# Kernel tuning notes

Hardware: AMD Instinct MI355X
Metric: run time of the kernel (lower is better)

## Reference

```python
import jax, jax.numpy as jnp
import numpy as np

B, D, H, C = 32768, 512, 512, 128  # batch, input_dim, hidden, n_classes (nurse==doctor)
L = 3  # 3 PAN layers and 3 shared FC layers
BN_EPS = 1e-5


def setup_inputs() -> dict:
    key = jax.random.key(0)
    ks = iter(jax.random.split(key, 64))

    def rn(shape, scale):
        return (jax.random.normal(next(ks), shape, jnp.float32) * scale)

    inv = lambda fan: 1.0 / np.sqrt(fan)

    x = jax.random.normal(next(ks), (B, D), jnp.float32)
    s_n = jax.random.randint(next(ks), (B,), 0, C)
    s_d = jax.random.randint(next(ks), (B,), 0, C)
    # cols -4 / -3 carry integer staffing caps (s_nurse_max, s_doctor_max)
    x = x.at[:, -4].set(s_n.astype(jnp.float32)).at[:, -3].set(s_d.astype(jnp.float32))

    inp = {
        'x': x,
        # ClinicalPAN params, stacked over L=3 layers (and 3 branches)
        'pbw': rn((L, 3, D, 32), inv(D)), 'pbb': jnp.zeros((L, 3, 32), jnp.float32),
        'paw1': rn((L, D, 64), inv(D)),  'pab1': jnp.zeros((L, 64), jnp.float32),
        'paw2': rn((L, 64, 32), inv(64)),'pab2': jnp.zeros((L, 32), jnp.float32),
        'piw1': rn((L, D, 16), inv(D)),  'pib1': jnp.zeros((L, 16), jnp.float32),
        'piw2': rn((L, 16, 1), inv(16)), 'pib2': jnp.zeros((L, 1), jnp.float32),
        'pfw': rn((L, 96, D), inv(96)),  'pfb': jnp.zeros((L, D), jnp.float32),
        'pgw': rn((L, D, D), inv(D)),    'pgb': jnp.zeros((L, D), jnp.float32),
        # shared Linear + BatchNorm1d (eval mode: running stats), stacked
        'fcw': rn((L, D, H), inv(D)),    'fcb': jnp.zeros((L, H), jnp.float32),
        'bng': jnp.ones((L, H), jnp.float32),  'bnb': jnp.zeros((L, H), jnp.float32),
        'bnm': jnp.zeros((L, H), jnp.float32), 'bnv': jnp.ones((L, H), jnp.float32),
        # heads
        'nhw1': rn((H, 64), inv(H)), 'nhb1': jnp.zeros((64,), jnp.float32),
        'nhw2': rn((64, C), inv(64)), 'nhb2': jnp.zeros((C,), jnp.float32),
        'dhw1': rn((H, 64), inv(H)), 'dhb1': jnp.zeros((64,), jnp.float32),
        'dhw2': rn((64, C), inv(64)), 'dhb2': jnp.zeros((C,), jnp.float32),
        'wtw1': rn((H, 64), inv(H)), 'wtb1': jnp.zeros((64,), jnp.float32),
        'wtw2': rn((64, 1), inv(64)), 'wtb2': jnp.zeros((1,), jnp.float32),
    }
    return inp


def reference(x, pbw, pbb, paw1, pab1, paw2, pab2, piw1, pib1, piw2, pib2,
              pfw, pfb, pgw, pgb, fcw, fcb, bng, bnb, bnm, bnv,
              nhw1, nhb1, nhw2, nhb2, dhw1, dhb1, dhw2, dhb2,
              wtw1, wtb1, wtw2, wtb2):
    # integer caps (constants w.r.t. grad)
    s_n = jax.lax.stop_gradient(x[:, -4]).astype(jnp.int32)
    s_d = jax.lax.stop_gradient(x[:, -3]).astype(jnp.int32)

    h = x
    for l in range(L):  # ClinicalPAN stack (dropout = identity in eval)
        cw = jax.nn.sigmoid(jax.nn.relu(h @ paw1[l] + pab1[l]) @ paw2[l] + pab2[l])   # [B,32]
        ci = jax.nn.sigmoid(jax.nn.relu(h @ piw1[l] + pib1[l]) @ piw2[l] + pib2[l])   # [B,1]
        feats = jax.nn.relu(jnp.einsum('bd,kdh->bkh', h, pbw[l]) + pbb[l][None])      # [B,3,32]
        weighted = feats * (cw * ci)[:, None, :]                                       # [B,3,32]
        fused = weighted.reshape(h.shape[0], 96) @ pfw[l] + pfb[l]                     # [B,D]
        gate = jax.nn.sigmoid(h @ pgw[l] + pgb[l])
        h = fused + gate * h

    for i in range(L):  # shared Linear -> BN(eval) -> ReLU
        z = h @ fcw[i] + fcb[i]
        z = bng[i] * (z - bnm[i]) * jax.lax.rsqrt(bnv[i] + BN_EPS) + bnb[i]
        h = jax.nn.relu(z)

    nurse_logits = jax.nn.relu(h @ nhw1 + nhb1) @ nhw2 + nhb2   # [B,C]
    doctor_logits = jax.nn.relu(h @ dhw1 + dhb1) @ dhw2 + dhb2  # [B,C]
    wait_time = jax.nn.relu(h @ wtw1 + wtb1) @ wtw2 + wtb2      # [B,1]

    idx = jnp.arange(C)
    nm = (idx[None, :] <= s_n[:, None]).astype(nurse_logits.dtype)
    dm = (idx[None, :] <= s_d[:, None]).astype(doctor_logits.dtype)
    NEG = jnp.asarray(-1e9, nurse_logits.dtype)
    nurse_logits = nurse_logits * nm + (1.0 - nm) * NEG
    doctor_logits = doctor_logits * dm + (1.0 - dm) * NEG
    return nurse_logits, doctor_logits, wait_time
```

## Files before the change

### kernel.cpp

```cpp
#include <hip/hip_runtime.h>

#define DI __device__ __forceinline__

typedef short bf16x8 __attribute__((ext_vector_type(8)));
typedef float f32x4  __attribute__((ext_vector_type(4)));

#define MFMA(a,b,c) __builtin_amdgcn_mfma_f32_16x16x32_bf16(a,b,c,0,0,0)

constexpr int    SZ_WT = 512*80;
constexpr int    SZ_WB = 512*96;
constexpr int    SZ_WF = 96*512;
constexpr int    SZ_WG = 512*512;
constexpr int    SZ_WC = 512*512;
constexpr size_t OFF_WT  = 0;
constexpr size_t OFF_WB  = OFF_WT + 3*(size_t)SZ_WT;
constexpr size_t OFF_WF  = OFF_WB + 3*(size_t)SZ_WB;
constexpr size_t OFF_WG  = OFF_WF + 3*(size_t)SZ_WF;
constexpr size_t OFF_WC  = OFF_WG + 3*(size_t)SZ_WG;
constexpr size_t OFF_WH  = OFF_WC + 3*(size_t)SZ_WC;
constexpr size_t OFF_WH2 = OFF_WH + (size_t)512*192;
constexpr size_t WS_TOTAL= OFF_WH2 + (size_t)128*256;

DI short f2b(float f){ unsigned u; __builtin_memcpy(&u,&f,4); u += 0x7fffu + ((u>>16)&1u); return (short)(u>>16); }
DI float b2f(short s){ unsigned u = ((unsigned)(unsigned short)s)<<16; float f; __builtin_memcpy(&f,&u,4); return f; }
DI float sigm(float x){ return 1.f/(1.f+__expf(-x)); }

__global__ __launch_bounds__(256) void prep_weights(
    const float* __restrict__ pbw,  const float* __restrict__ paw1,
    const float* __restrict__ piw1, const float* __restrict__ pfw,
    const float* __restrict__ pgw,  const float* __restrict__ fcw,
    const float* __restrict__ nhw1, const float* __restrict__ nhw2,
    const float* __restrict__ dhw1, const float* __restrict__ dhw2,
    const float* __restrict__ wtw1, short* __restrict__ ws)
{
  size_t t = (size_t)blockIdx.x*256 + threadIdx.x;
  if (t >= WS_TOTAL) return;
  float v = 0.f;
  if (t < OFF_WB) {
    int q=(int)t; int ly=q/SZ_WT; int qq=q%SZ_WT;
    int j=qq&7, lane=(qq>>3)&63, tile=qq>>9, kt=tile&15, nt=tile>>4;
    int k=kt*32+((lane>>4)<<3)+j, n=nt*16+(lane&15);
    v = (n<64) ? paw1[((size_t)ly*512+k)*64+n] : piw1[((size_t)ly*512+k)*16+(n-64)];
  } else if (t < OFF_WF) {
    int q=(int)(t-OFF_WB); int ly=q/SZ_WB; int qq=q%SZ_WB;
    int j=qq&7, lane=(qq>>3)&63, tile=qq>>9, kt=tile&15, nt=tile>>4;
    int k=kt*32+((lane>>4)<<3)+j, c=nt*16+(lane&15);
    v = pbw[(((size_t)ly*3+(c>>5))*512+k)*32+(c&31)];
  } else if (t < OFF_WG) {
    int q=(int)(t-OFF_WF); int ly=q/SZ_WF; int qq=q%SZ_WF;
    int j=qq&7, lane=(qq>>3)&63, tile=qq>>9, kt=tile%3, nt=tile/3;
    int k=kt*32+((lane>>4)<<3)+j, n=nt*16+(lane&15);
    v = pfw[((size_t)ly*96+k)*512+n];
  } else if (t < OFF_WC) {
    int q=(int)(t-OFF_WG); int ly=q/SZ_WG; int qq=q%SZ_WG;
    int j=qq&7, lane=(qq>>3)&63, tile=qq>>9, kt=tile&15, nt=tile>>4;
    int k=kt*32+((lane>>4)<<3)+j, n=nt*16+(lane&15);
    v = pgw[((size_t)ly*512+k)*512+n];
  } else if (t < OFF_WH) {
    int q=(int)(t-OFF_WC); int ly=q/SZ_WC; int qq=q%SZ_WC;
    int j=qq&7, lane=(qq>>3)&63, tile=qq>>9, kt=tile&15, nt=tile>>4;
    int k=kt*32+((lane>>4)<<3)+j, n=nt*16+(lane&15);
    v = fcw[((size_t)ly*512+k)*512+n];
  } else if (t < OFF_WH2) {
    int qq=(int)(t-OFF_WH);
    int j=qq&7, lane=(qq>>3)&63, tile=qq>>9, kt=tile&15, nt=tile>>4;
    int k=kt*32+((lane>>4)<<3)+j, n=nt*16+(lane&15);
    v = (n<64) ? nhw1[(size_t)k*64+n] : (n<128) ? dhw1[(size_t)k*64+(n-64)] : wtw1[(size_t)k*64+(n-128)];
  } else {
    int qq=(int)(t-OFF_WH2);
    int j=qq&7, lane=(qq>>3)&63, tile=qq>>9, kt=tile&3, nt=tile>>2;
    int k=kt*32+((lane>>4)<<3)+j, n=nt*16+(lane&15);
    if (k<64) v = (n<128) ? nhw2[(size_t)k*128+n] : 0.f;
    else      v = (n>=128)? dhw2[(size_t)(k-64)*128+(n-128)] : 0.f;
  }
  ws[t] = f2b(v);
}

__global__ __launch_bounds__(512, 4) void pan_main(
  const float* __restrict__ x,
  const float* __restrict__ pbb,  const float* __restrict__ pab1,
  const float* __restrict__ paw2, const float* __restrict__ pab2,
  const float* __restrict__ pib1, const float* __restrict__ piw2,
  const float* __restrict__ pib2, const float* __restrict__ pfb,
  const float* __restrict__ pgb,  const float* __restrict__ fcb,
  const float* __restrict__ bng,  const float* __restrict__ bnb,
  const float* __restrict__ bnm,  const float* __restrict__ bnv,
  const float* __restrict__ nhb1, const float* __restrict__ nhb2,
  const float* __restrict__ dhb1, const float* __restrict__ dhb2,
  const float* __restrict__ wtb1, const float* __restrict__ wtw2,
  const float* __restrict__ wtb2,
  const short* __restrict__ ws, float* __restrict__ out)
{
  __shared__ __align__(16) char lds[81920];
  char* hA = lds;
  char* hB = lds + 32768;
  char* sU = lds + 65536;
  char* sW = lds + 73728;

  const int tid  = threadIdx.x;
  const int wave = tid >> 6;
  const int l    = tid & 63;
  const int lr   = l & 15;
  const int lb   = l >> 4;
  const int swzA = (lr & 7) << 4;
  const size_t row0 = (size_t)blockIdx.x * 32;

  #pragma unroll 2
  for (int c = tid; c < 2048; c += 512) {
    int row = c >> 6, k0 = (c & 63) << 3;
    const float4* s0 = (const float4*)(x + (row0 + row)*512 + k0);
    float4 f0 = s0[0], f1 = s0[1];
    bf16x8 p;
    p[0]=f2b(f0.x); p[1]=f2b(f0.y); p[2]=f2b(f0.z); p[3]=f2b(f0.w);
    p[4]=f2b(f1.x); p[5]=f2b(f1.y); p[6]=f2b(f1.z); p[7]=f2b(f1.w);
    *(bf16x8*)(hA + row*1024 + ((k0*2) ^ ((row&7)<<4))) = p;
  }
  __syncthreads();

  auto ldA = [&](const char* base, int rt, int kt) -> bf16x8 {
    int row = rt*16 + lr;
    return *(const bf16x8*)(base + row*1024 + ((kt*64 + lb*16) ^ swzA));
  };
  auto ldB = [&](const short* W, int K32, int nt, int kt) -> bf16x8 {
    return *(const bf16x8*)(W + (((size_t)(nt*K32 + kt))*64 + l)*8);
  };
  auto ldH = [&](const char* base, int row, int col) -> float {
    return b2f(*(const short*)(base + row*1024 + ((col*2) ^ ((row&7)<<4))));
  };
  auto stH = [&](char* base, int row, int col, float v) {
    *(short*)(base + row*1024 + ((col*2) ^ ((row&7)<<4))) = f2b(v);
  };
  const f32x4 FZ = {0.f,0.f,0.f,0.f};

  for (int ly = 0; ly < 3; ++ly) {
    if (wave < 5) {
      const short* W = ws + OFF_WT + (size_t)ly*SZ_WT;
      f32x4 acc[2];
      #pragma unroll
      for (int rt=0;rt<2;++rt) acc[rt] = FZ;
      #pragma unroll 2
      for (int kt=0;kt<16;++kt) {
        bf16x8 b = ldB(W,16,wave,kt);
        #pragma unroll
        for (int rt=0;rt<2;++rt) acc[rt] = MFMA(ldA(hA,rt,kt), b, acc[rt]);
      }
      const int col = wave*16 + lr;
      const float bias = (col<64) ? pab1[ly*64+col] : pib1[ly*16+(col-64)];
      #pragma unroll
      for (int rt=0;rt<2;++rt)
        #pragma unroll
        for (int jj=0;jj<4;++jj) {
          int row = rt*16 + lb*4 + jj;
          *(short*)(sU + row*160 + col*2) = f2b(fmaxf(acc[rt][jj]+bias, 0.f));
        }
    }
    __syncthreads();
    if (tid < 32) {
      float s = pib2[ly];
      bf16x8 t0 = *(const bf16x8*)(sU + tid*160 + 128);
      bf16x8 t1 = *(const bf16x8*)(sU + tid*160 + 144);
      #pragma unroll
      for (int i=0;i<8;++i) {
        s += b2f(t0[i]) * piw2[ly*16+i];
        s += b2f(t1[i]) * piw2[ly*16+8+i];
      }
      *(float*)(sU + 5120 + tid*4) = sigm(s);
    }
    __syncthreads();
    {
      const int r = tid>>4, j0 = (tid&15)<<1;
      float a2[2];
      a2[0] = pab2[ly*32 + j0];
      a2[1] = pab2[ly*32 + j0 + 1];
      #pragma unroll 2
      for (int k8=0;k8<8;++k8) {
        bf16x8 tv8 = *(const bf16x8*)(sU + r*160 + k8*16);
        #pragma unroll
        for (int i8=0;i8<8;++i8) {
          float tv = b2f(tv8[i8]);
          float2 wr = *(const float2*)(paw2 + ((size_t)ly*64 + k8*8+i8)*32 + j0);
          a2[0]=fmaf(tv,wr.x,a2[0]); a2[1]=fmaf(tv,wr.y,a2[1]);
        }
      }
      const float civ = *(const float*)(sU + 5120 + r*4);
      *(short*)(sU + 5248 + (r*32 + j0    )*2) = f2b(sigm(a2[0]) * civ);
      *(short*)(sU + 5248 + (r*32 + j0 + 1)*2) = f2b(sigm(a2[1]) * civ);
    }
    __syncthreads();
    if (wave < 6) {
      const short* W = ws + OFF_WB + (size_t)ly*SZ_WB;
      f32x4 acc[2];
      #pragma unroll
      for (int rt=0;rt<2;++rt) acc[rt] = FZ;
      #pragma unroll 2
      for (int kt=0;kt<16;++kt) {
        bf16x8 b = ldB(W,16,wave,kt);
        #pragma unroll
        for (int rt=0;rt<2;++rt) acc[rt] = MFMA(ldA(hA,rt,kt), b, acc[rt]);
      }
      const int col = wave*16 + lr;
      const float bias = pbb[ly*96 + col];
      #pragma unroll
      for (int rt=0;rt<2;++rt)
        #pragma unroll
        for (int jj=0;jj<4;++jj) {
          int row = rt*16 + lb*4 + jj;
          float cc = b2f(*(const short*)(sU + 5248 + (row*32 + (col&31))*2));
          float wv = fmaxf(acc[rt][jj]+bias, 0.f) * cc;
          *(short*)(sW + row*256 + ((col*2) ^ ((row&7)<<4))) = f2b(wv);
        }
    }
    __syncthreads();
    {
      const short* Wg = ws + OFF_WG + (size_t)ly*SZ_WG;
      const short* Wf = ws + OFF_WF + (size_t)ly*SZ_WF;
      #pragma unroll 1
      for (int c=0; c<4; ++c) {
        f32x4 acc[2];
        #pragma unroll
        for (int rt=0;rt<2;++rt) acc[rt] = FZ;
        #pragma unroll 2
        for (int kt=0;kt<16;++kt) {
          bf16x8 b = ldB(Wg,16, wave*4+c, kt);
          #pragma unroll
          for (int rt=0;rt<2;++rt) acc[rt] = MFMA(ldA(hA,rt,kt), b, acc[rt]);
        }
        const int col = (wave*4+c)*16 + lr;
        const float gb = pgb[ly*512+col];
        const float fb = pfb[ly*512+col];
        #pragma unroll
        for (int rt=0;rt<2;++rt)
          #pragma unroll
          for (int jj=0;jj<4;++jj) {
            int row = rt*16 + lb*4 + jj;
            acc[rt][jj] = sigm(acc[rt][jj]+gb)*ldH(hA,row,col) + fb;
          }
        #pragma unroll 1
        for (int kt=0;kt<3;++kt) {
          bf16x8 b = ldB(Wf,3, wave*4+c, kt);
          #pragma unroll
          for (int rt=0;rt<2;++rt) {
            int row = rt*16 + lr;
            bf16x8 a = *(const bf16x8*)(sW + row*256 + ((kt*64 + lb*16) ^ swzA));
            acc[rt] = MFMA(a,b,acc[rt]);
          }
        }
        #pragma unroll
        for (int rt=0;rt<2;++rt)
          #pragma unroll
          for (int jj=0;jj<4;++jj)
            stH(hB, rt*16 + lb*4 + jj, col, acc[rt][jj]);
      }
    }
    __syncthreads();
    { char* t = hA; hA = hB; hB = t; }
  }

  for (int fi=0; fi<3; ++fi) {
    const short* W = ws + OFF_WC + (size_t)fi*SZ_WC;
    #pragma unroll 1
    for (int c=0; c<4; ++c) {
      f32x4 acc[2];
      #pragma unroll
      for (int rt=0;rt<2;++rt) acc[rt] = FZ;
      #pragma unroll 2
      for (int kt=0;kt<16;++kt) {
        bf16x8 b = ldB(W,16, wave*4+c, kt);
        #pragma unroll
        for (int rt=0;rt<2;++rt) acc[rt] = MFMA(ldA(hA,rt,kt), b, acc[rt]);
      }
      const int col = (wave*4+c)*16 + lr;
      const float sc = bng[fi*512+col] * rsqrtf(bnv[fi*512+col] + 1e-5f);
      const float of = bnb[fi*512+col] - bnm[fi*512+col]*sc;
      const float bb = fcb[fi*512+col];
      #pragma unroll
      for (int rt=0;rt<2;++rt)
        #pragma unroll
        for (int jj=0;jj<4;++jj)
          stH(hB, rt*16 + lb*4 + jj, col,
              fmaxf((acc[rt][jj] + bb)*sc + of, 0.f));
    }
    __syncthreads();
    { char* t = hA; hA = hB; hB = t; }
  }

  {
    const short* W = ws + OFF_WH;
    {
      f32x4 acc[2];
      #pragma unroll
      for (int rt=0;rt<2;++rt) acc[rt] = FZ;
      #pragma unroll 2
      for (int kt=0;kt<16;++kt) {
        bf16x8 b = ldB(W,16,wave,kt);
        #pragma unroll
        for (int rt=0;rt<2;++rt) acc[rt] = MFMA(ldA(hA,rt,kt), b, acc[rt]);
      }
      const int col = wave*16 + lr;
      const float bias = (col<64) ? nhb1[col] : dhb1[col-64];
      #pragma unroll
      for (int rt=0;rt<2;++rt)
        #pragma unroll
        for (int jj=0;jj<4;++jj) {
          int row = rt*16 + lb*4 + jj;
          *(short*)(hB + row*384 + ((col*2) ^ ((row&7)<<4))) =
              f2b(fmaxf(acc[rt][jj]+bias, 0.f));
        }
    }
    if (wave < 4) {
      f32x4 acc[2];
      #pragma unroll
      for (int rt=0;rt<2;++rt) acc[rt] = FZ;
      #pragma unroll 2
      for (int kt=0;kt<16;++kt) {
        bf16x8 b = ldB(W,16, 8+wave, kt);
        #pragma unroll
        for (int rt=0;rt<2;++rt) acc[rt] = MFMA(ldA(hA,rt,kt), b, acc[rt]);
      }
      const int col = (8+wave)*16 + lr;
      const float bias = wtb1[col-128];
      #pragma unroll
      for (int rt=0;rt<2;++rt)
        #pragma unroll
        for (int jj=0;jj<4;++jj) {
          int row = rt*16 + lb*4 + jj;
          *(short*)(hB + row*384 + ((col*2) ^ ((row&7)<<4))) =
              f2b(fmaxf(acc[rt][jj]+bias, 0.f));
        }
    }
  }
  __syncthreads();
  {
    const short* W2 = ws + OFF_WH2;
    #pragma unroll 1
    for (int p=0;p<2;++p) {
      f32x4 acc[2];
      #pragma unroll
      for (int rt=0;rt<2;++rt) acc[rt] = FZ;
      #pragma unroll 2
      for (int kt=0;kt<4;++kt) {
        bf16x8 b = ldB(W2,4, wave*2+p, kt);
        #pragma unroll
        for (int rt=0;rt<2;++rt) {
          int row = rt*16 + lr;
          bf16x8 a = *(const bf16x8*)(hB + row*384 + ((kt*64 + lb*16) ^ swzA));
          acc[rt] = MFMA(a,b,acc[rt]);
        }
      }
      const int col2 = (wave*2+p)*16 + lr;
      const bool isn = col2 < 128;
      const int cc = col2 & 127;
      const float bias = isn ? nhb2[cc] : dhb2[cc];
      const size_t obase = isn ? (size_t)0 : (size_t)4194304;
      #pragma unroll
      for (int rt=0;rt<2;++rt)
        #pragma unroll
        for (int jj=0;jj<4;++jj) {
          int row = rt*16 + lb*4 + jj;
          size_t rg = row0 + row;
          float2 caps = *(const float2*)(x + rg*512 + 508);
          int cap = (int)(isn ? caps.x : caps.y);
          float v = acc[rt][jj] + bias;
          out[obase + rg*128 + cc] = (cc <= cap) ? v : -1e9f;
        }
    }
  }
  if (tid < 32) {
    float s = wtb2[0];
    #pragma unroll 2
    for (int k8=0;k8<8;++k8) {
      bf16x8 hv = *(const bf16x8*)(hB + tid*384 + ((256 + k8*16) ^ ((tid&7)<<4)));
      #pragma unroll
      for (int i=0;i<8;++i) s += b2f(hv[i]) * wtw2[k8*8+i];
    }
    out[(size_t)8388608 + row0 + tid] = s;
  }
}

extern "C" void kernel_launch(void* const* d_in, const int* in_sizes, int n_in,
                              void* d_out, int out_size, void* d_ws, size_t ws_size,
                              hipStream_t stream) {
  const float* x    = (const float*)d_in[0];
  const float* pbw  = (const float*)d_in[1];
  const float* pbb  = (const float*)d_in[2];
  const float* paw1 = (const float*)d_in[3];
  const float* pab1 = (const float*)d_in[4];
  const float* paw2 = (const float*)d_in[5];
  const float* pab2 = (const float*)d_in[6];
  const float* piw1 = (const float*)d_in[7];
  const float* pib1 = (const float*)d_in[8];
  const float* piw2 = (const float*)d_in[9];
  const float* pib2 = (const float*)d_in[10];
  const float* pfw  = (const float*)d_in[11];
  const float* pfb  = (const float*)d_in[12];
  const float* pgw  = (const float*)d_in[13];
  const float* pgb  = (const float*)d_in[14];
  const float* fcw  = (const float*)d_in[15];
  const float* fcb  = (const float*)d_in[16];
  const float* bng  = (const float*)d_in[17];
  const float* bnb  = (const float*)d_in[18];
  const float* bnm  = (const float*)d_in[19];
  const float* bnv  = (const float*)d_in[20];
  const float* nhw1 = (const float*)d_in[21];
  const float* nhb1 = (const float*)d_in[22];
  const float* nhw2 = (const float*)d_in[23];
  const float* nhb2 = (const float*)d_in[24];
  const float* dhw1 = (const float*)d_in[25];
  const float* dhb1 = (const float*)d_in[26];
  const float* dhw2 = (const float*)d_in[27];
  const float* dhb2 = (const float*)d_in[28];
  const float* wtw1 = (const float*)d_in[29];
  const float* wtb1 = (const float*)d_in[30];
  const float* wtw2 = (const float*)d_in[31];
  const float* wtb2 = (const float*)d_in[32];
  short* ws  = (short*)d_ws;
  float* out = (float*)d_out;

  prep_weights<<<(int)((WS_TOTAL + 255)/256), 256, 0, stream>>>(
      pbw, paw1, piw1, pfw, pgw, fcw, nhw1, nhw2, dhw1, dhw2, wtw1, ws);
  pan_main<<<1024, 512, 0, stream>>>(
      x, pbb, pab1, paw2, pab2, pib1, piw2, pib2, pfb, pgb, fcb,
      bng, bnb, bnm, bnv, nhb1, nhb2, dhb1, dhb2, wtb1, wtw2, wtb2, ws, out);
}
```

Before: 382.8 us.

## Double workgroup size to 1024 threads and redistribute MFMA tiles across 16 waves

Each block now runs 1024 threads (16 waves) over the same 32 rows instead of 512. The small PAN projections are split by row-half so more waves take part, the 512-wide gate and FC GEMMs give each wave 2 column tiles instead of 4, and the head layers get one tile per wave. The goal is more parallelism and latency hiding inside each block while keeping per-block LDS the same. The risk is fewer resident blocks per CU because of register limits at 1024 threads, and B-weight tiles being loaded redundantly by both row-half waves in the small GEMMs.

Result: faster. 329.4 us (-13.9%).

```diff
diff --git a/kernel.cpp b/kernel.cpp
--- a/kernel.cpp
+++ b/kernel.cpp
@@ -76,7 +76,7 @@
   ws[t] = f2b(v);
 }
 
-__global__ __launch_bounds__(512, 4) void pan_main(
+__global__ __launch_bounds__(1024, 4) void pan_main(
   const float* __restrict__ x,
   const float* __restrict__ pbb,  const float* __restrict__ pab1,
   const float* __restrict__ paw2, const float* __restrict__ pab2,
@@ -106,7 +106,7 @@
   const size_t row0 = (size_t)blockIdx.x * 32;
 
   #pragma unroll 2
-  for (int c = tid; c < 2048; c += 512) {
+  for (int c = tid; c < 2048; c += 1024) {
     int row = c >> 6, k0 = (c & 63) << 3;
     const float4* s0 = (const float4*)(x + (row0 + row)*512 + k0);
     float4 f0 = s0[0], f1 = s0[1];
@@ -133,26 +133,22 @@
   const f32x4 FZ = {0.f,0.f,0.f,0.f};
 
   for (int ly = 0; ly < 3; ++ly) {
-    if (wave < 5) {
+    if (wave < 10) {
       const short* W = ws + OFF_WT + (size_t)ly*SZ_WT;
-      f32x4 acc[2];
-      #pragma unroll
-      for (int rt=0;rt<2;++rt) acc[rt] = FZ;
+      const int nt = wave % 5, rh = wave / 5;
+      f32x4 acc = FZ;
       #pragma unroll 2
       for (int kt=0;kt<16;++kt) {
-        bf16x8 b = ldB(W,16,wave,kt);
-        #pragma unroll
-        for (int rt=0;rt<2;++rt) acc[rt] = MFMA(ldA(hA,rt,kt), b, acc[rt]);
-      }
-      const int col = wave*16 + lr;
+        bf16x8 b = ldB(W,16,nt,kt);
+        acc = MFMA(ldA(hA,rh,kt), b, acc);
+      }
+      const int col = nt*16 + lr;
       const float bias = (col<64) ? pab1[ly*64+col] : pib1[ly*16+(col-64)];
       #pragma unroll
-      for (int rt=0;rt<2;++rt)
-        #pragma unroll
-        for (int jj=0;jj<4;++jj) {
-          int row = rt*16 + lb*4 + jj;
-          *(short*)(sU + row*160 + col*2) = f2b(fmaxf(acc[rt][jj]+bias, 0.f));
-        }
+      for (int jj=0;jj<4;++jj) {
+        int row = rh*16 + lb*4 + jj;
+        *(short*)(sU + row*160 + col*2) = f2b(fmaxf(acc[jj]+bias, 0.f));
+      }
     }
     __syncthreads();
     if (tid < 32) {
@@ -168,64 +164,55 @@
     }
     __syncthreads();
     {
-      const int r = tid>>4, j0 = (tid&15)<<1;
-      float a2[2];
-      a2[0] = pab2[ly*32 + j0];
-      a2[1] = pab2[ly*32 + j0 + 1];
+      const int r = tid>>5, j0 = tid&31;
+      float a = pab2[ly*32 + j0];
       #pragma unroll 2
       for (int k8=0;k8<8;++k8) {
         bf16x8 tv8 = *(const bf16x8*)(sU + r*160 + k8*16);
         #pragma unroll
-        for (int i8=0;i8<8;++i8) {
-          float tv = b2f(tv8[i8]);
-          float2 wr = *(const float2*)(paw2 + ((size_t)ly*64 + k8*8+i8)*32 + j0);
-          a2[0]=fmaf(tv,wr.x,a2[0]); a2[1]=fmaf(tv,wr.y,a2[1]);
-        }
+        for (int i8=0;i8<8;++i8)
+          a = fmaf(b2f(tv8[i8]), paw2[((size_t)ly*64 + k8*8+i8)*32 + j0], a);
       }
       const float civ = *(const float*)(sU + 5120 + r*4);
-      *(short*)(sU + 5248 + (r*32 + j0    )*2) = f2b(sigm(a2[0]) * civ);
-      *(short*)(sU + 5248 + (r*32 + j0 + 1)*2) = f2b(sigm(a2[1]) * civ);
-    }
-    __syncthreads();
-    if (wave < 6) {
+      *(short*)(sU + 5248 + (r*32 + j0)*2) = f2b(sigm(a) * civ);
+    }
+    __syncthreads();
+    if (wave < 12) {
       const short* W = ws + OFF_WB + (size_t)ly*SZ_WB;
-      f32x4 acc[2];
-      #pragma unroll
-      for (int rt=0;rt<2;++rt) acc[rt] = FZ;
+      const int nt = wave % 6, rh = wave / 6;
+      f32x4 acc = FZ;
       #pragma unroll 2
       for (int kt=0;kt<16;++kt) {
-        bf16x8 b = ldB(W,16,wave,kt);
-        #pragma unroll
-        for (int rt=0;rt<2;++rt) acc[rt] = MFMA(ldA(hA,rt,kt), b, acc[rt]);
-      }
-      const int col = wave*16 + lr;
+        bf16x8 b = ldB(W,16,nt,kt);
+        acc = MFMA(ldA(hA,rh,kt), b, acc);
+      }
+      const int col = nt*16 + lr;
       const float bias = pbb[ly*96 + col];
       #pragma unroll
-      for (int rt=0;rt<2;++rt)
-        #pragma unroll
-        for (int jj=0;jj<4;++jj) {
-          int row = rt*16 + lb*4 + jj;
-          float cc = b2f(*(const short*)(sU + 5248 + (row*32 + (col&31))*2));
-          float wv = fmaxf(acc[rt][jj]+bias, 0.f) * cc;
-          *(short*)(sW + row*256 + ((col*2) ^ ((row&7)<<4))) = f2b(wv);
-        }
+      for (int jj=0;jj<4;++jj) {
+        int row = rh*16 + lb*4 + jj;
+        float cc = b2f(*(const short*)(sU + 5248 + (row*32 + (col&31))*2));
+        float wv = fmaxf(acc[jj]+bias, 0.f) * cc;
+        *(short*)(sW + row*256 + ((col*2) ^ ((row&7)<<4))) = f2b(wv);
+      }
     }
     __syncthreads();
     {
       const short* Wg = ws + OFF_WG + (size_t)ly*SZ_WG;
       const short* Wf = ws + OFF_WF + (size_t)ly*SZ_WF;
       #pragma unroll 1
-      for (int c=0; c<4; ++c) {
+      for (int c=0; c<2; ++c) {
+        const int ct = wave*2 + c;
         f32x4 acc[2];
         #pragma unroll
         for (int rt=0;rt<2;++rt) acc[rt] = FZ;
         #pragma unroll 2
         for (int kt=0;kt<16;++kt) {
-          bf16x8 b = ldB(Wg,16, wave*4+c, kt);
+          bf16x8 b = ldB(Wg,16, ct, kt);
           #pragma unroll
           for (int rt=0;rt<2;++rt) acc[rt] = MFMA(ldA(hA,rt,kt), b, acc[rt]);
         }
-        const int col = (wave*4+c)*16 + lr;
+        const int col = ct*16 + lr;
         const float gb = pgb[ly*512+col];
         const float fb = pfb[ly*512+col];
         #pragma unroll
@@ -237,7 +224,7 @@
           }
         #pragma unroll 1
         for (int kt=0;kt<3;++kt) {
-          bf16x8 b = ldB(Wf,3, wave*4+c, kt);
+          bf16x8 b = ldB(Wf,3, ct, kt);
           #pragma unroll
           for (int rt=0;rt<2;++rt) {
             int row = rt*16 + lr;
@@ -259,17 +246,18 @@
   for (int fi=0; fi<3; ++fi) {
     const short* W = ws + OFF_WC + (size_t)fi*SZ_WC;
     #pragma unroll 1
-    for (int c=0; c<4; ++c) {
+    for (int c=0; c<2; ++c) {
+      const int ct = wave*2 + c;
       f32x4 acc[2];
       #pragma unroll
       for (int rt=0;rt<2;++rt) acc[rt] = FZ;
       #pragma unroll 2
       for (int kt=0;kt<16;++kt) {
-        bf16x8 b = ldB(W,16, wave*4+c, kt);
+        bf16x8 b = ldB(W,16, ct, kt);
         #pragma unroll
         for (int rt=0;rt<2;++rt) acc[rt] = MFMA(ldA(hA,rt,kt), b, acc[rt]);
       }
-      const int col = (wave*4+c)*16 + lr;
+      const int col = ct*16 + lr;
       const float sc = bng[fi*512+col] * rsqrtf(bnv[fi*512+col] + 1e-5f);
       const float of = bnb[fi*512+col] - bnm[fi*512+col]*sc;
       const float bb = fcb[fi*512+col];
@@ -284,86 +272,60 @@
     { char* t = hA; hA = hB; hB = t; }
   }
 
-  {
+  if (wave < 12) {
     const short* W = ws + OFF_WH;
-    {
-      f32x4 acc[2];
-      #pragma unroll
-      for (int rt=0;rt<2;++rt) acc[rt] = FZ;
-      #pragma unroll 2
-      for (int kt=0;kt<16;++kt) {
-        bf16x8 b = ldB(W,16,wave,kt);
-        #pragma unroll
-        for (int rt=0;rt<2;++rt) acc[rt] = MFMA(ldA(hA,rt,kt), b, acc[rt]);
-      }
-      const int col = wave*16 + lr;
-      const float bias = (col<64) ? nhb1[col] : dhb1[col-64];
-      #pragma unroll
-      for (int rt=0;rt<2;++rt)
-        #pragma unroll
-        for (int jj=0;jj<4;++jj) {
-          int row = rt*16 + lb*4 + jj;
-          *(short*)(hB + row*384 + ((col*2) ^ ((row&7)<<4))) =
-              f2b(fmaxf(acc[rt][jj]+bias, 0.f));
-        }
-    }
-    if (wave < 4) {
-      f32x4 acc[2];
-      #pragma unroll
-      for (int rt=0;rt<2;++rt) acc[rt] = FZ;
-      #pragma unroll 2
-      for (int kt=0;kt<16;++kt) {
-        bf16x8 b = ldB(W,16, 8+wave, kt);
-        #pragma unroll
-        for (int rt=0;rt<2;++rt) acc[rt] = MFMA(ldA(hA,rt,kt), b, acc[rt]);
-      }
-      const int col = (8+wave)*16 + lr;
-      const float bias = wtb1[col-128];
-      #pragma unroll
-      for (int rt=0;rt<2;++rt)
-        #pragma unroll
-        for (int jj=0;jj<4;++jj) {
-          int row = rt*16 + lb*4 + jj;
-          *(short*)(hB + row*384 + ((col*2) ^ ((row&7)<<4))) =
-              f2b(fmaxf(acc[rt][jj]+bias, 0.f));
-        }
-    }
+    f32x4 acc[2];
+    #pragma unroll
+    for (int rt=0;rt<2;++rt) acc[rt] = FZ;
+    #pragma unroll 2
+    for (int kt=0;kt<16;++kt) {
+      bf16x8 b = ldB(W,16,wave,kt);
+      #pragma unroll
+      for (int rt=0;rt<2;++rt) acc[rt] = MFMA(ldA(hA,rt,kt), b, acc[rt]);
+    }
+    const int col = wave*16 + lr;
+    const float bias = (col<64) ? nhb1[col] : (col<128) ? dhb1[col-64] : wtb1[col-128];
+    #pragma unroll
+    for (int rt=0;rt<2;++rt)
+      #pragma unroll
+      for (int jj=0;jj<4;++jj) {
+        int row = rt*16 + lb*4 + jj;
+        *(short*)(hB + row*384 + ((col*2) ^ ((row&7)<<4))) =
+            f2b(fmaxf(acc[rt][jj]+bias, 0.f));
+      }
   }
   __syncthreads();
   {
     const short* W2 = ws + OFF_WH2;
-    #pragma unroll 1
-    for (int p=0;p<2;++p) {
-      f32x4 acc[2];
-      #pragma unroll
-      for (int rt=0;rt<2;++rt) acc[rt] = FZ;
-      #pragma unroll 2
-      for (int kt=0;kt<4;++kt) {
-        bf16x8 b = ldB(W2,4, wave*2+p, kt);
-        #pragma unroll
-        for (int rt=0;rt<2;++rt) {
-          int row = rt*16 + lr;
-          bf16x8 a = *(const bf16x8*)(hB + row*384 + ((kt*64 + lb*16) ^ swzA));
-          acc[rt] = MFMA(a,b,acc[rt]);
-        }
-      }
-      const int col2 = (wave*2+p)*16 + lr;
-      const bool isn = col2 < 128;
-      const int cc = col2 & 127;
-      const float bias = isn ? nhb2[cc] : dhb2[cc];
-      const size_t obase = isn ? (size_t)0 : (size_t)4194304;
-      #pragma unroll
-      for (int rt=0;rt<2;++rt)
-        #pragma unroll
-        for (int jj=0;jj<4;++jj) {
-          int row = rt*16 + lb*4 + jj;
-          size_t rg = row0 + row;
-          float2 caps = *(const float2*)(x + rg*512 + 508);
-          int cap = (int)(isn ? caps.x : caps.y);
-          float v = acc[rt][jj] + bias;
-          out[obase + rg*128 + cc] = (cc <= cap) ? v : -1e9f;
-        }
-    }
+    f32x4 acc[2];
+    #pragma unroll
+    for (int rt=0;rt<2;++rt) acc[rt] = FZ;
+    #pragma unroll 2
+    for (int kt=0;kt<4;++kt) {
+      bf16x8 b = ldB(W2,4, wave, kt);
+      #pragma unroll
+      for (int rt=0;rt<2;++rt) {
+        int row = rt*16 + lr;
+        bf16x8 a = *(const bf16x8*)(hB + row*384 + ((kt*64 + lb*16) ^ swzA));
+        acc[rt] = MFMA(a,b,acc[rt]);
+      }
+    }
+    const int col2 = wave*16 + lr;
+    const bool isn = col2 < 128;
+    const int cc = col2 & 127;
+    const float bias = isn ? nhb2[cc] : dhb2[cc];
+    const size_t obase = isn ? (size_t)0 : (size_t)4194304;
+    #pragma unroll
+    for (int rt=0;rt<2;++rt)
+      #pragma unroll
+      for (int jj=0;jj<4;++jj) {
+        int row = rt*16 + lb*4 + jj;
+        size_t rg = row0 + row;
+        float2 caps = *(const float2*)(x + rg*512 + 508);
+        int cap = (int)(isn ? caps.x : caps.y);
+        float v = acc[rt][jj] + bias;
+        out[obase + rg*128 + cc] = (cc <= cap) ? v : -1e9f;
+      }
   }
   if (tid < 32) {
     float s = wtb2[0];
@@ -418,7 +380,7 @@
 
   prep_weights<<<(int)((WS_TOTAL + 255)/256), 256, 0, stream>>>(
       pbw, paw1, piw1, pfw, pgw, fcw, nhw1, nhw2, dhw1, dhw2, wtw1, ws);
-  pan_main<<<1024, 512, 0, stream>>>(
+  pan_main<<<1024, 1024, 0, stream>>>(
       x, pbb, pab1, paw2, pab2, pib1, piw2, pib2, pfb, pgb, fcb,
       bng, bnb, bnm, bnv, nhb1, nhb2, dhb1, dhb2, wtb1, wtw2, wtb2, ws, out);
 }
```
